# Kernel tuning notes

Measured on AMD Instinct MI355X. Metric: run time of the kernel, lower is better.

Reference implementation:

```python
import jax, jax.numpy as jnp
import numpy as np

IN_DIM = 64
OUT_DIM = 64
SPLINE_ORDER = 3
GRID_SIZE = 8
GRID_LOW, GRID_HIGH = -1.0, 1.0
BATCH = 2048


def generate_control_points(low, high, in_dim, out_dim, spline_order, grid_size):
    # Knot vector extended spline_order points beyond the range on each side.
    spacing = (high - low) / grid_size
    knots = jnp.arange(-spline_order, grid_size + spline_order + 1, dtype=jnp.float32) * spacing + low
    # (out_dim, in_dim, grid_size + 2*spline_order + 1)
    return jnp.broadcast_to(knots, (out_dim, in_dim, knots.shape[0]))


def compute_bspline(x, grid, k):
    """Cox-de Boor recursion.
    x:    (B, in_dim)
    grid: (out_dim, in_dim, G + 2k + 1)
    returns bases: (B, out_dim, in_dim, G + k)
    """
    xe = x[:, None, :, None]  # (B, 1, in, 1)
    g = grid[None]            # (1, out, in, n_knots)
    bases = ((xe >= g[..., :-1]) & (xe < g[..., 1:])).astype(x.dtype)
    for j in range(1, k + 1):
        left = (xe - g[..., : -(j + 1)]) / (g[..., j:-1] - g[..., : -(j + 1)])
        right = (g[..., j + 1 :] - xe) / (g[..., j + 1 :] - g[..., 1:-j])
        bases = left * bases[..., :-1] + right * bases[..., 1:]
    return bases


def setup_inputs() -> dict:
    key = jax.random.key(0)
    kx, kc = jax.random.split(key)
    x = jax.random.normal(kx, (BATCH, IN_DIM), dtype=jnp.float32)
    grid = generate_control_points(GRID_LOW, GRID_HIGH, IN_DIM, OUT_DIM, SPLINE_ORDER, GRID_SIZE)
    # xavier_normal_ on (out, in, G+k): fan_in = in*(G+k), fan_out = out*(G+k)
    n_coef = GRID_SIZE + SPLINE_ORDER
    std = float(np.sqrt(2.0 / (IN_DIM * n_coef + OUT_DIM * n_coef)))
    coef = jax.random.normal(kc, (OUT_DIM, IN_DIM, n_coef), dtype=jnp.float32) * std
    return {"x": x, "grid": grid, "coef": coef}


def reference(x, grid, coef):
    bases = compute_bspline(x, grid, SPLINE_ORDER)        # (B, out, in, G+k)
    spline = jnp.sum(bases * coef[None], axis=-1)          # (B, out, in)
    return spline
```

## Files before the change

### kernel.cpp

```cpp
#include <hip/hip_runtime.h>


#define BATCH    2048
#define IN_DIM   64
#define OUT_DIM  64
#define NCOEF    11
#define B_TILE   32
#define B_SUB    8
#define O_TILE   8
#define NPAIR    (B_SUB * IN_DIM)
#define PLANE    (NPAIR * 4)
#define CTILE    (O_TILE * IN_DIM * NCOEF)

__global__ __launch_bounds__(256) void kan_kernel(
    const float* __restrict__ x,
    const float* __restrict__ grid,
    const float* __restrict__ coef,
    float* __restrict__ out)
{
    __shared__ float bas_lds[3 * PLANE];
    __shared__ float coef_lds[CTILE];

    const int tid    = threadIdx.x;
    const int o_tile = blockIdx.x & (OUT_DIM / O_TILE - 1);
    const int b0     = (blockIdx.x >> 3) * B_TILE;

    const float* csrc = coef + (size_t)o_tile * CTILE;
    #pragma unroll
    for (int q = 0; q < CTILE / 256; ++q)
        coef_lds[tid + q * 256] = csrc[tid + q * 256];

    const float g0    = grid[0];
    const float inv_h = 1.0f / (grid[1] - g0);

    __syncthreads();

    const int i   = tid & 63;
    const int grp = tid >> 6;
    const int ol0 = grp * 2;
    const int o   = o_tile * O_TILE + ol0;

    float c[2][NCOEF];
    #pragma unroll
    for (int oo = 0; oo < 2; ++oo) {
        const int row = ((ol0 + oo) * IN_DIM + i) * NCOEF;
        #pragma unroll
        for (int t = 0; t < NCOEF; ++t)
            c[oo][t] = coef_lds[row + t];
    }

    for (int sub = 0; sub < B_TILE / B_SUB; ++sub) {
        const int r0 = b0 + sub * B_SUB;

        #pragma unroll
        for (int qq = 0; qq < NPAIR / 256; ++qq) {
            const int p  = tid + qq * 256;
            const float xv = x[(size_t)(r0 + (p >> 6)) * IN_DIM + (p & 63)];

            const float4 z = make_float4(0.f, 0.f, 0.f, 0.f);
            *(float4*)&bas_lds[0 * PLANE + p * 4] = z;
            *(float4*)&bas_lds[1 * PLANE + p * 4] = z;
            *(float4*)&bas_lds[2 * PLANE + p * 4] = z;

            const float pos = (xv - g0) * inv_h;
            if (pos >= 0.0f && pos < 14.0f) {
                const int   m  = (int)pos;
                const float t  = pos - (float)m;
                const float t2 = t * t;
                const float t3 = t2 * t;
                const float s  = 1.0f - t;
                const float w0 = s * s * s * (1.0f / 6.0f);
                const float w1 = (3.0f * t3 - 6.0f * t2 + 4.0f) * (1.0f / 6.0f);
                const float w2 = (-3.0f * t3 + 3.0f * t2 + 3.0f * t + 1.0f) * (1.0f / 6.0f);
                const float w3 = t3 * (1.0f / 6.0f);

                const int mb = m - 3;
                int idx;
                idx = mb + 0; if ((unsigned)idx < NCOEF) bas_lds[(idx >> 2) * PLANE + p * 4 + (idx & 3)] = w0;
                idx = mb + 1; if ((unsigned)idx < NCOEF) bas_lds[(idx >> 2) * PLANE + p * 4 + (idx & 3)] = w1;
                idx = mb + 2; if ((unsigned)idx < NCOEF) bas_lds[(idx >> 2) * PLANE + p * 4 + (idx & 3)] = w2;
                idx = mb + 3; if ((unsigned)idx < NCOEF) bas_lds[(idx >> 2) * PLANE + p * 4 + (idx & 3)] = w3;
            }
        }
        __syncthreads();

        #pragma unroll
        for (int rr = 0; rr < B_SUB; ++rr) {
            const int p = rr * IN_DIM + i;
            const float4 v0 = *(const float4*)&bas_lds[0 * PLANE + p * 4];
            const float4 v1 = *(const float4*)&bas_lds[1 * PLANE + p * 4];
            const float4 v2 = *(const float4*)&bas_lds[2 * PLANE + p * 4];

            float* op = &out[(size_t)(r0 + rr) * (OUT_DIM * IN_DIM) + o * IN_DIM + i];
            #pragma unroll
            for (int oo = 0; oo < 2; ++oo) {
                float acc;
                acc  = v0.x * c[oo][0] + v0.y * c[oo][1] + v0.z * c[oo][2] + v0.w * c[oo][3];
                acc += v1.x * c[oo][4] + v1.y * c[oo][5] + v1.z * c[oo][6] + v1.w * c[oo][7];
                acc += v2.x * c[oo][8] + v2.y * c[oo][9] + v2.z * c[oo][10];
                op[oo * IN_DIM] = acc;
            }
        }
        __syncthreads();
    }
}

extern "C" void kernel_launch(void* const* d_in, const int* in_sizes, int n_in,
                              void* d_out, int out_size, void* d_ws, size_t ws_size,
                              hipStream_t stream) {
    const float* x    = (const float*)d_in[0];
    const float* grid = (const float*)d_in[1];
    const float* coef = (const float*)d_in[2];
    float* out = (float*)d_out;

    const int nblocks = (BATCH / B_TILE) * (OUT_DIM / O_TILE);
    kan_kernel<<<nblocks, 256, 0, stream>>>(x, grid, coef, out);
}
```

Before: 17.33 us.

## Restructure into 1024-thread blocks covering half the outputs with single-pass basis

Each block now uses 1024 threads and covers 16 batch rows against half of the output dimension (32 outputs), where before it used 256 threads for 32 rows by 8 outputs. The basis for the block's rows is computed once in a single pass, which removes the inner sub-batch loop and its two barriers per iteration. The x load is issued before the coefficient staging so the two overlap. In exchange, each block stages a much larger coefficient tile (about 88KB of LDS), which limits how many blocks can sit on a CU. Coefficient staging also moves from 4 KB per 8 output rows to 88 KB per 16 batch rows, raising the total staged coefficient traffic.

```diff
diff --git a/kernel.cpp b/kernel.cpp
--- a/kernel.cpp
+++ b/kernel.cpp
@@ -5,40 +5,68 @@
 #define IN_DIM   64
 #define OUT_DIM  64
 #define NCOEF    11
-#define B_TILE   32
-#define B_SUB    8
-#define O_TILE   8
-#define NPAIR    (B_SUB * IN_DIM)
+#define B_TILE   16
+#define O_HALF   32
+#define NPAIR    (B_TILE * IN_DIM)
 #define PLANE    (NPAIR * 4)
-#define CTILE    (O_TILE * IN_DIM * NCOEF)
+#define CTILE    (O_HALF * IN_DIM * NCOEF)
 
-__global__ __launch_bounds__(256) void kan_kernel(
+__global__ __launch_bounds__(1024) void kan_kernel(
     const float* __restrict__ x,
     const float* __restrict__ grid,
     const float* __restrict__ coef,
     float* __restrict__ out)
 {
+    __shared__ float coef_lds[CTILE];
     __shared__ float bas_lds[3 * PLANE];
-    __shared__ float coef_lds[CTILE];
 
     const int tid    = threadIdx.x;
-    const int o_tile = blockIdx.x & (OUT_DIM / O_TILE - 1);
-    const int b0     = (blockIdx.x >> 3) * B_TILE;
+    const int o_half = blockIdx.x & 1;
+    const int b0     = (blockIdx.x >> 1) * B_TILE;
 
-    const float* csrc = coef + (size_t)o_tile * CTILE;
+    const int p = tid;
+    const float xv = x[(size_t)(b0 + (p >> 6)) * IN_DIM + (p & 63)];
+
+    const float* csrc = coef + (size_t)o_half * CTILE;
     #pragma unroll
-    for (int q = 0; q < CTILE / 256; ++q)
-        coef_lds[tid + q * 256] = csrc[tid + q * 256];
+    for (int q = 0; q < CTILE / 1024; ++q)
+        coef_lds[tid + q * 1024] = csrc[tid + q * 1024];
 
     const float g0    = grid[0];
     const float inv_h = 1.0f / (grid[1] - g0);
 
+    {
+        const float4 z = make_float4(0.f, 0.f, 0.f, 0.f);
+        *(float4*)&bas_lds[0 * PLANE + p * 4] = z;
+        *(float4*)&bas_lds[1 * PLANE + p * 4] = z;
+        *(float4*)&bas_lds[2 * PLANE + p * 4] = z;
+
+        const float pos = (xv - g0) * inv_h;
+        if (pos >= 0.0f && pos < 14.0f) {
+            const int   m  = (int)pos;
+            const float t  = pos - (float)m;
+            const float t2 = t * t;
+            const float t3 = t2 * t;
+            const float s  = 1.0f - t;
+            const float w0 = s * s * s * (1.0f / 6.0f);
+            const float w1 = (3.0f * t3 - 6.0f * t2 + 4.0f) * (1.0f / 6.0f);
+            const float w2 = (-3.0f * t3 + 3.0f * t2 + 3.0f * t + 1.0f) * (1.0f / 6.0f);
+            const float w3 = t3 * (1.0f / 6.0f);
+
+            const int mb = m - 3;
+            int idx;
+            idx = mb + 0; if ((unsigned)idx < NCOEF) bas_lds[(idx >> 2) * PLANE + p * 4 + (idx & 3)] = w0;
+            idx = mb + 1; if ((unsigned)idx < NCOEF) bas_lds[(idx >> 2) * PLANE + p * 4 + (idx & 3)] = w1;
+            idx = mb + 2; if ((unsigned)idx < NCOEF) bas_lds[(idx >> 2) * PLANE + p * 4 + (idx & 3)] = w2;
+            idx = mb + 3; if ((unsigned)idx < NCOEF) bas_lds[(idx >> 2) * PLANE + p * 4 + (idx & 3)] = w3;
+        }
+    }
     __syncthreads();
 
     const int i   = tid & 63;
     const int grp = tid >> 6;
     const int ol0 = grp * 2;
-    const int o   = o_tile * O_TILE + ol0;
+    const int o   = o_half * O_HALF + ol0;
 
     float c[2][NCOEF];
     #pragma unroll
@@ -49,59 +77,23 @@
             c[oo][t] = coef_lds[row + t];
     }
 
-    for (int sub = 0; sub < B_TILE / B_SUB; ++sub) {
-        const int r0 = b0 + sub * B_SUB;
+    float* op0 = &out[(size_t)b0 * (OUT_DIM * IN_DIM) + o * IN_DIM + i];
+    #pragma unroll 4
+    for (int rr = 0; rr < B_TILE; ++rr) {
+        const int pp = rr * IN_DIM + i;
+        const float4 v0 = *(const float4*)&bas_lds[0 * PLANE + pp * 4];
+        const float4 v1 = *(const float4*)&bas_lds[1 * PLANE + pp * 4];
+        const float4 v2 = *(const float4*)&bas_lds[2 * PLANE + pp * 4];
 
+        float* op = op0 + (size_t)rr * (OUT_DIM * IN_DIM);
         #pragma unroll
-        for (int qq = 0; qq < NPAIR / 256; ++qq) {
-            const int p  = tid + qq * 256;
-            const float xv = x[(size_t)(r0 + (p >> 6)) * IN_DIM + (p & 63)];
-
-            const float4 z = make_float4(0.f, 0.f, 0.f, 0.f);
-            *(float4*)&bas_lds[0 * PLANE + p * 4] = z;
-            *(float4*)&bas_lds[1 * PLANE + p * 4] = z;
-            *(float4*)&bas_lds[2 * PLANE + p * 4] = z;
-
-            const float pos = (xv - g0) * inv_h;
-            if (pos >= 0.0f && pos < 14.0f) {
-                const int   m  = (int)pos;
-                const float t  = pos - (float)m;
-                const float t2 = t * t;
-                const float t3 = t2 * t;
-                const float s  = 1.0f - t;
-                const float w0 = s * s * s * (1.0f / 6.0f);
-                const float w1 = (3.0f * t3 - 6.0f * t2 + 4.0f) * (1.0f / 6.0f);
-                const float w2 = (-3.0f * t3 + 3.0f * t2 + 3.0f * t + 1.0f) * (1.0f / 6.0f);
-                const float w3 = t3 * (1.0f / 6.0f);
-
-                const int mb = m - 3;
-                int idx;
-                idx = mb + 0; if ((unsigned)idx < NCOEF) bas_lds[(idx >> 2) * PLANE + p * 4 + (idx & 3)] = w0;
-                idx = mb + 1; if ((unsigned)idx < NCOEF) bas_lds[(idx >> 2) * PLANE + p * 4 + (idx & 3)] = w1;
-                idx = mb + 2; if ((unsigned)idx < NCOEF) bas_lds[(idx >> 2) * PLANE + p * 4 + (idx & 3)] = w2;
-                idx = mb + 3; if ((unsigned)idx < NCOEF) bas_lds[(idx >> 2) * PLANE + p * 4 + (idx & 3)] = w3;
-            }
+        for (int oo = 0; oo < 2; ++oo) {
+            float acc;
+            acc  = v0.x * c[oo][0] + v0.y * c[oo][1] + v0.z * c[oo][2] + v0.w * c[oo][3];
+            acc += v1.x * c[oo][4] + v1.y * c[oo][5] + v1.z * c[oo][6] + v1.w * c[oo][7];
+            acc += v2.x * c[oo][8] + v2.y * c[oo][9] + v2.z * c[oo][10];
+            op[oo * IN_DIM] = acc;
         }
-        __syncthreads();
-
-        #pragma unroll
-        for (int rr = 0; rr < B_SUB; ++rr) {
-            const int p = rr * IN_DIM + i;
-            const float4 v0 = *(const float4*)&bas_lds[0 * PLANE + p * 4];
-            const float4 v1 = *(const float4*)&bas_lds[1 * PLANE + p * 4];
-            const float4 v2 = *(const float4*)&bas_lds[2 * PLANE + p * 4];
-
-            float* op = &out[(size_t)(r0 + rr) * (OUT_DIM * IN_DIM) + o * IN_DIM + i];
-            #pragma unroll
-            for (int oo = 0; oo < 2; ++oo) {
-                float acc;
-                acc  = v0.x * c[oo][0] + v0.y * c[oo][1] + v0.z * c[oo][2] + v0.w * c[oo][3];
-                acc += v1.x * c[oo][4] + v1.y * c[oo][5] + v1.z * c[oo][6] + v1.w * c[oo][7];
-                acc += v2.x * c[oo][8] + v2.y * c[oo][9] + v2.z * c[oo][10];
-                op[oo * IN_DIM] = acc;
-            }
-        }
-        __syncthreads();
     }
 }
 
@@ -113,6 +105,6 @@
     const float* coef = (const float*)d_in[2];
     float* out = (float*)d_out;
 
-    const int nblocks = (BATCH / B_TILE) * (OUT_DIM / O_TILE);
-    kan_kernel<<<nblocks, 256, 0, stream>>>(x, grid, coef, out);
+    const int nblocks = (BATCH / B_TILE) * 2;
+    kan_kernel<<<nblocks, 1024, 0, stream>>>(x, grid, coef, out);
 }
```

Result: faster. 14.42 us (-16.8%).
